# Kernel optimization log

Measured on AMD Instinct MI355X. Metric: run time of the kernel, lower is better.

## Reference

```python
import jax, jax.numpy as jnp
import numpy as np

B, S, E, D, L, H = 8, 1024, 512, 1024, 8, 16
HD = D // H                 # 64
ROT = max(HD // 2, 32)      # 32
FF = 4 * D
FUSED = 3 * D + 2 * FF      # q,k,v,ff,ff_gate
EPS = 1e-5


def layer_norm(x, w, b):
    mu = jnp.mean(x, axis=-1, keepdims=True)
    var = jnp.mean(jnp.square(x - mu), axis=-1, keepdims=True)
    return (x - mu) * jax.lax.rsqrt(var + EPS) * w + b


def gelu(x):  # fused_gelu from source (erf form, constant 1.41421)
    return x * 0.5 * (1.0 + jax.scipy.special.erf(x / 1.41421))


def silu(x):
    return x * jax.nn.sigmoid(x)


def rotate_half(x):
    x1, x2 = jnp.split(x, 2, axis=-1)
    return jnp.concatenate([-x2, x1], axis=-1)


def rope_tables(seq_len):
    inv = 1.0 / (10000.0 ** (jnp.arange(0, ROT, 2, dtype=jnp.float32) / ROT))
    freqs = jnp.arange(seq_len, dtype=jnp.float32)[:, None] * inv[None, :]
    emb = jnp.concatenate([freqs, freqs], axis=-1)  # [S, ROT]
    # source caches sin/cos in bfloat16 (precision=torch.bfloat16)
    sin = jnp.sin(emb).astype(jnp.bfloat16).astype(jnp.float32)[None, None]
    cos = jnp.cos(emb).astype(jnp.bfloat16).astype(jnp.float32)[None, None]
    return sin, cos  # [1,1,S,ROT]


def setup_inputs() -> dict:
    key = jax.random.key(0)
    ks = jax.random.split(key, 24)
    std = 0.02
    inp = {
        "noisy_embeds": jax.random.normal(ks[0], (B, S, E), jnp.float32),
        "cond_embeds": jax.random.normal(ks[1], (B, S, E), jnp.float32),
        "prev_embeds": jax.random.normal(ks[2], (B, S, E), jnp.float32),
        "infill_mask": jax.random.uniform(ks[3], (B, S, 1), jnp.float32),
        "attention_mask": jnp.zeros((B, 1, 1, S), jnp.float32),
        "times": jax.random.uniform(ks[4], (B,), jnp.float32),
        # time embedding params
        "fourier_w": jax.random.normal(ks[5], (D // 2, 1), jnp.float32),
        "t1_w": jax.random.normal(ks[6], (D, D), jnp.float32) * std,
        "t1_b": jnp.zeros((D,), jnp.float32),
        "t2_w": jax.random.normal(ks[7], (D, D), jnp.float32) * std,
        "t2_b": jnp.zeros((D,), jnp.float32),
        # input projection
        "in_w": jax.random.normal(ks[8], (D, 4 * E), jnp.float32) * std,
        "in_b": jnp.zeros((D,), jnp.float32),
        # per-layer (stacked) block params
        "ln_w": jnp.ones((L, D), jnp.float32),
        "ln_b": jnp.zeros((L, D), jnp.float32),
        "cond_w": jax.random.normal(ks[9], (L, 2 * D, D), jnp.float32) * std,
        "cond_b": jnp.zeros((L, 2 * D), jnp.float32),
        "proj_w": jax.random.normal(ks[10], (L, FUSED, D), jnp.float32) * std,
        "attn_w": jax.random.normal(ks[11], (L, D, D), jnp.float32) * std,
        "attn_b": jnp.zeros((L, D), jnp.float32),
        "ff_w": jax.random.normal(ks[12], (L, D, FF), jnp.float32) * std,
        "ff_b": jnp.zeros((L, D), jnp.float32),
        # output head
        "outln_w": jnp.ones((D,), jnp.float32),
        "outln_b": jnp.zeros((D,), jnp.float32),
        "out_w": jax.random.normal(ks[13], (E, D), jnp.float32) * std,
        "out_b": jnp.zeros((E,), jnp.float32),
        "fin_w": jnp.ones((E,), jnp.float32),
        "fin_b": jnp.zeros((E,), jnp.float32),
    }
    return inp


def _split_heads(x):  # [B,S,H*hd] -> [B,H,S,hd]
    return x.reshape(B, S, H, HD).transpose(0, 2, 1, 3)


def _forward(noisy_embeds, cond_embeds, prev_embeds, infill_mask, attention_mask,
             times, fourier_w, t1_w, t1_b, t2_w, t2_b, in_w, in_b,
             ln_w, ln_b, cond_w, cond_b, proj_w, attn_w, attn_b, ff_w, ff_b,
             outln_w, outln_b, out_w, out_b, fin_w, fin_b):
    # -- time embedding (Random Fourier + MLP) --
    f = 2.0 * np.pi * (times[:, None] @ fourier_w.T)          # [B, D/2]
    te = jnp.concatenate([jnp.cos(f), jnp.sin(f)], axis=-1)   # [B, D]
    te = gelu(te @ t1_w.T + t1_b) @ t2_w.T + t2_b             # [B, D]
    time_embeds = te[:, None, :]                              # [B, 1, D]

    # -- input projection: cat(noisy, cond, prev, mask broadcast) --
    mask_feat = infill_mask * jnp.ones_like(noisy_embeds)     # [B,S,E]
    x = jnp.concatenate([noisy_embeds, cond_embeds, prev_embeds, mask_feat], axis=-1)
    h = x @ in_w.T + in_b                                     # [B,S,D]

    sin, cos = rope_tables(S)
    sm_scale = HD ** (-0.5)

    for i in range(L):
        units = layer_norm(h, ln_w[i], ln_b[i])
        # FiLM conditioning
        sb = silu(time_embeds) @ cond_w[i].T + cond_b[i]      # [B,1,2D]
        scale, bias = jnp.split(sb, 2, axis=-1)
        units = (1.0 + scale) * units + bias
        # fused projection and split
        proj = units @ proj_w[i].T                            # [B,S,11D]
        q, k, v, ff, ff_gate = jnp.split(
            proj, np.cumsum([D, D, D, FF])[:4].tolist(), axis=-1)
        q, k, v = _split_heads(q), _split_heads(k), _split_heads(v)  # [B,H,S,hd]
        # rotary on first ROT dims
        q = jnp.concatenate(
            [q[..., :ROT] * cos + rotate_half(q[..., :ROT]) * sin, q[..., ROT:]], axis=-1)
        k = jnp.concatenate(
            [k[..., :ROT] * cos + rotate_half(k[..., :ROT]) * sin, k[..., ROT:]], axis=-1)
        # NOTE: source scales BOTH q and k by hd^-0.5 (effective hd^-1)
        score = jnp.einsum('bhsd,bhSd->bhsS', q * sm_scale, k * sm_scale)
        score = score + attention_mask
        w = jax.nn.softmax(score, axis=-1)
        attn = jnp.einsum('bhsS,bhSd->bhsd', w, v)
        merged = attn.transpose(0, 2, 1, 3).reshape(B, S, D)
        attn_out = merged @ attn_w[i].T + attn_b[i]
        ff_out = (ff * gelu(ff_gate)) @ ff_w[i].T + ff_b[i]
        h = h + attn_out + ff_out

    out = layer_norm(h, outln_w, outln_b) @ out_w.T + out_b   # [B,S,E]
    return layer_norm(out, fin_w, fin_b)


def reference(noisy_embeds, cond_embeds, prev_embeds, infill_mask, attention_mask,
              times, fourier_w, t1_w, t1_b, t2_w, t2_b, in_w, in_b,
              ln_w, ln_b, cond_w, cond_b, proj_w, attn_w, attn_b, ff_w, ff_b,
              outln_w, outln_b, out_w, out_b, fin_w, fin_b):
    return _forward(noisy_embeds, cond_embeds, prev_embeds, infill_mask, attention_mask,
                    times, fourier_w, t1_w, t1_b, t2_w, t2_b, in_w, in_b,
                    ln_w, ln_b, cond_w, cond_b, proj_w, attn_w, attn_b, ff_w, ff_b,
                    outln_w, outln_b, out_w, out_b, fin_w, fin_b)
```

## Files before the change

### kernel.cpp

```cpp
#include <hip/hip_runtime.h>
#include <hip/hip_bf16.h>
#include <cstddef>
#include <cstdint>

#define BB 8
#define SS 1024
#define EE 512
#define DD 1024
#define LL 8
#define HH 16
#define HD 64
#define ROT 32
#define FF 4096
#define FUSED 11264
#define NTOK 8192
#define QKVW 3072

using u16 = unsigned short;
typedef __attribute__((ext_vector_type(8))) __bf16 bf16x8;
typedef __attribute__((ext_vector_type(4))) float f32x4;
typedef __attribute__((ext_vector_type(4))) unsigned short u16x4;
typedef __attribute__((ext_vector_type(8))) unsigned short u16x8;

typedef const __attribute__((address_space(1))) void gas_t;
typedef __attribute__((address_space(3))) void las_t;

__device__ __forceinline__ void gld16(const void* g, void* l) {
  __builtin_amdgcn_global_load_lds((gas_t*)g, (las_t*)l, 16, 0, 0);
}

__device__ __forceinline__ float bf2f(u16 u) {
  union { unsigned int i; float f; } v; v.i = ((unsigned int)u) << 16; return v.f;
}
__device__ __forceinline__ u16 f2bf(float f) {
  union { float f; unsigned int i; } v; v.f = f;
  unsigned int u = v.i;
  unsigned int r = u + 0x7FFFu + ((u >> 16) & 1u);
  return (u16)(r >> 16);
}
__device__ __forceinline__ float gelu_f(float x) {
  return x * 0.5f * (1.0f + erff(x / 1.41421f));
}
__device__ __forceinline__ float silu_f(float x) {
  return x / (1.0f + __expf(-x));
}

template <int ACCUM, int OUTBF16, int GATED>
__global__ __launch_bounds__(256, 2) void gemm_bt(
    const u16* __restrict__ A, const u16* __restrict__ W,
    const float* __restrict__ bias, void* __restrict__ Cp,
    int M, int N, int K) {
  __shared__ __align__(16) u16 As[2][128 * 64];
  __shared__ __align__(16) u16 Bs[2][128 * 64];
  const int tid = threadIdx.x;
  const int w = tid >> 6, lane = tid & 63;
  const int m0 = blockIdx.y * 128, n0 = blockIdx.x * 128;
  const int wm = w >> 1, wn = w & 1;

  f32x4 acc[4][4] = {};

  auto stage = [&](int buf, int k0) {
#pragma unroll
    for (int i = 0; i < 4; i++) {
      const int c = w + i * 4;
      const int r = c * 8 + (lane >> 3);
      const int colb = ((lane & 7) << 4) ^ ((r & 7) << 4);
      gld16(A + (size_t)(m0 + r) * K + k0 + (colb >> 1), &As[buf][c * 512]);
      gld16(W + (size_t)(n0 + r) * K + k0 + (colb >> 1), &Bs[buf][c * 512]);
    }
  };

  stage(0, 0);
  __syncthreads();

  for (int k0 = 0; k0 < K; k0 += 64) {
    const int cur = (k0 >> 6) & 1;
    if (k0 + 64 < K) stage(cur ^ 1, k0 + 64);

    __builtin_amdgcn_s_setprio(1);
#pragma unroll
    for (int ks = 0; ks < 2; ks++) {
      bf16x8 av[4], bv[4];
#pragma unroll
      for (int m = 0; m < 4; m++) {
        const int row = wm * 64 + m * 16 + (lane & 15);
        const int cb = (ks * 64 + ((lane >> 4) << 4)) ^ ((row & 7) << 4);
        av[m] = *(const bf16x8*)((const char*)As[cur] + row * 128 + cb);
      }
#pragma unroll
      for (int n = 0; n < 4; n++) {
        const int row = wn * 64 + n * 16 + (lane & 15);
        const int cb = (ks * 64 + ((lane >> 4) << 4)) ^ ((row & 7) << 4);
        bv[n] = *(const bf16x8*)((const char*)Bs[cur] + row * 128 + cb);
      }
#pragma unroll
      for (int m = 0; m < 4; m++)
#pragma unroll
        for (int n = 0; n < 4; n++)
          acc[m][n] = __builtin_amdgcn_mfma_f32_16x16x32_bf16(av[m], bv[n], acc[m][n], 0, 0, 0);
    }
    __builtin_amdgcn_s_setprio(0);
    __syncthreads();
  }

  const int rowb0 = m0 + wm * 64 + ((lane >> 4) << 2);
  if (GATED) {
    const int No = N >> 1;
#pragma unroll
    for (int n = 0; n < 4; n += 2) {
      const int outcol = (n0 >> 1) + wn * 32 + ((n >> 1) << 4) + (lane & 15);
#pragma unroll
      for (int m = 0; m < 4; m++)
#pragma unroll
        for (int r = 0; r < 4; r++) {
          const float fv = acc[m][n][r];
          const float gv = acc[m][n + 1][r];
          ((u16*)Cp)[(size_t)(rowb0 + m * 16 + r) * No + outcol] = f2bf(fv * gelu_f(gv));
        }
    }
    return;
  }
  const int colb0 = n0 + wn * 64 + (lane & 15);
#pragma unroll
  for (int n = 0; n < 4; n++) {
    const int col = colb0 + n * 16;
    const float bn = bias ? bias[col] : 0.0f;
#pragma unroll
    for (int m = 0; m < 4; m++) {
#pragma unroll
      for (int r = 0; r < 4; r++) {
        const size_t idx = (size_t)(rowb0 + m * 16 + r) * N + col;
        const float v = acc[m][n][r] + bn;
        if (ACCUM) {
          ((float*)Cp)[idx] += v;
        } else if (OUTBF16) {
          ((u16*)Cp)[idx] = f2bf(v);
        } else {
          ((float*)Cp)[idx] = v;
        }
      }
    }
  }
}

__global__ __launch_bounds__(256, 2) void attn_fwd(
    const u16* __restrict__ qr, const u16* __restrict__ kr,
    const u16* __restrict__ vt, const float* __restrict__ mask,
    u16* __restrict__ merged) {
  __shared__ __align__(16) u16 Ks[2][128 * 64];
  __shared__ __align__(16) u16 Vs[2][64 * 128];
  __shared__ __align__(16) u16 Ps[4][16 * 128];
  const int tid = threadIdx.x, w = tid >> 6, lane = tid & 63;
  const int g = blockIdx.x;
  const int j = g >> 3;
  const int bh = (g & 7) + ((j >> 4) << 3);
  const int qx = j & 15;
  const int b = bh >> 4;
  const int q0 = qx * 64 + w * 16;
  const u16* Qb = qr + (size_t)bh * SS * HD;
  const u16* Kb = kr + (size_t)bh * SS * HD;
  const u16* Vb = vt + (size_t)bh * HD * SS;
  const float* mb = mask + (size_t)b * SS;

  bf16x8 qf0, qf1;
  {
    const int qrow = q0 + (lane & 15);
    const u16* qp = Qb + (size_t)qrow * HD + ((lane >> 4) << 3);
    qf0 = *(const bf16x8*)qp;
    qf1 = *(const bf16x8*)(qp + 32);
  }

  float mrun[4], srun[4];
  f32x4 acc[4] = {};
#pragma unroll
  for (int r = 0; r < 4; r++) { mrun[r] = -1e30f; srun[r] = 0.0f; }

  u16* pw = &Ps[w][0];

  auto stage = [&](int buf, int kv0) {
#pragma unroll
    for (int i = 0; i < 4; i++) {
      const int c = w + i * 4;
      {
        const int r = c * 8 + (lane >> 3);
        const int colb = ((lane & 7) << 4) ^ ((r & 7) << 4);
        gld16(Kb + (size_t)(kv0 + r) * HD + (colb >> 1), &Ks[buf][c * 512]);
      }
      {
        const int d = c * 4 + (lane >> 4);
        const int colb = ((lane & 15) << 4) ^ ((d & 7) << 4);
        gld16(Vb + (size_t)d * SS + kv0 + (colb >> 1), &Vs[buf][c * 512]);
      }
    }
  };

  stage(0, 0);
  __syncthreads();

  for (int t = 0; t < 8; t++) {
    const int cur = t & 1;
    const int kv0 = t * 128;
    if (t < 7) stage(cur ^ 1, kv0 + 128);

    f32x4 p[8];
    __builtin_amdgcn_s_setprio(1);
#pragma unroll
    for (int blk = 0; blk < 8; blk++) {
      const int row = blk * 16 + (lane & 15);
      const int swz = (row & 7) << 4;
      const bf16x8 k0v = *(const bf16x8*)((const char*)Ks[cur] + row * 128 + ((((lane >> 4) << 4)) ^ swz));
      const bf16x8 k1v = *(const bf16x8*)((const char*)Ks[cur] + row * 128 + ((64 + ((lane >> 4) << 4)) ^ swz));
      f32x4 z = {};
      p[blk] = __builtin_amdgcn_mfma_f32_16x16x32_bf16(qf0, k0v, z, 0, 0, 0);
      p[blk] = __builtin_amdgcn_mfma_f32_16x16x32_bf16(qf1, k1v, p[blk], 0, 0, 0);
    }
    __builtin_amdgcn_s_setprio(0);

    float mv[8];
#pragma unroll
    for (int blk = 0; blk < 8; blk++) mv[blk] = mb[kv0 + blk * 16 + (lane & 15)];
#pragma unroll
    for (int blk = 0; blk < 8; blk++)
#pragma unroll
      for (int r = 0; r < 4; r++) p[blk][r] = p[blk][r] * (1.0f / 64.0f) + mv[blk];

    float fac[4];
#pragma unroll
    for (int r = 0; r < 4; r++) {
      float tm = p[0][r];
#pragma unroll
      for (int blk = 1; blk < 8; blk++) tm = fmaxf(tm, p[blk][r]);
      tm = fmaxf(tm, __shfl_xor(tm, 1));
      tm = fmaxf(tm, __shfl_xor(tm, 2));
      tm = fmaxf(tm, __shfl_xor(tm, 4));
      tm = fmaxf(tm, __shfl_xor(tm, 8));
      const float mn = fmaxf(mrun[r], tm);
      fac[r] = __expf(mrun[r] - mn);
      mrun[r] = mn;
      float rs = 0.0f;
#pragma unroll
      for (int blk = 0; blk < 8; blk++) {
        const float e = __expf(p[blk][r] - mn);
        p[blk][r] = e;
        rs += e;
      }
      rs += __shfl_xor(rs, 1);
      rs += __shfl_xor(rs, 2);
      rs += __shfl_xor(rs, 4);
      rs += __shfl_xor(rs, 8);
      srun[r] = srun[r] * fac[r] + rs;
    }
#pragma unroll
    for (int dblk = 0; dblk < 4; dblk++)
#pragma unroll
      for (int r = 0; r < 4; r++) acc[dblk][r] *= fac[r];

#pragma unroll
    for (int blk = 0; blk < 8; blk++)
#pragma unroll
      for (int r = 0; r < 4; r++) {
        const int q = ((lane >> 4) << 2) + r;
        pw[(q * 128 + blk * 16 + (lane & 15)) ^ ((q & 7) << 3)] = f2bf(p[blk][r]);
      }

    bf16x8 pa[4];
#pragma unroll
    for (int ks = 0; ks < 4; ks++) {
      const int q = lane & 15;
      pa[ks] = *(const bf16x8*)(pw + ((q * 128 + ks * 32 + ((lane >> 4) << 3)) ^ ((q & 7) << 3)));
    }

    __builtin_amdgcn_s_setprio(1);
#pragma unroll
    for (int dblk = 0; dblk < 4; dblk++) {
      const int drow = dblk * 16 + (lane & 15);
      const int swz = (drow & 7) << 4;
#pragma unroll
      for (int ks = 0; ks < 4; ks++) {
        const bf16x8 vv = *(const bf16x8*)((const char*)Vs[cur] + drow * 256 + ((ks * 64 + ((lane >> 4) << 4)) ^ swz));
        acc[dblk] = __builtin_amdgcn_mfma_f32_16x16x32_bf16(pa[ks], vv, acc[dblk], 0, 0, 0);
      }
    }
    __builtin_amdgcn_s_setprio(0);

    __syncthreads();
  }

#pragma unroll
  for (int dblk = 0; dblk < 4; dblk++)
#pragma unroll
    for (int r = 0; r < 4; r++) {
      const int sq = q0 + ((lane >> 4) << 2) + r;
      const int d = dblk * 16 + (lane & 15);
      merged[((size_t)b * SS + sq) * DD + (bh & 15) * HD + d] = f2bf(acc[dblk][r] / srun[r]);
    }
}

__global__ __launch_bounds__(256) void ln_mod(
    const float* __restrict__ x, const float* __restrict__ lw,
    const float* __restrict__ lb, const float* __restrict__ sb,
    u16* __restrict__ out) {
  const int row = blockIdx.x, tid = threadIdx.x;
  const float4 v = ((const float4*)(x + (size_t)row * DD))[tid];
  float vv[4] = {v.x, v.y, v.z, v.w};
  float s = vv[0] + vv[1] + vv[2] + vv[3];
  float q = vv[0] * vv[0] + vv[1] * vv[1] + vv[2] * vv[2] + vv[3] * vv[3];
  for (int off = 1; off < 64; off <<= 1) {
    s += __shfl_xor(s, off);
    q += __shfl_xor(q, off);
  }
  __shared__ float red[8];
  const int w = tid >> 6, lane = tid & 63;
  if (lane == 0) { red[w] = s; red[4 + w] = q; }
  __syncthreads();
  s = red[0] + red[1] + red[2] + red[3];
  q = red[4] + red[5] + red[6] + red[7];
  const float mu = s * (1.0f / DD);
  const float inv = rsqrtf(q * (1.0f / DD) - mu * mu + 1e-5f);
  const int b = row >> 10;
  u16x4 o;
#pragma unroll
  for (int j = 0; j < 4; j++) {
    const int d = tid * 4 + j;
    float g = (vv[j] - mu) * inv * lw[d] + lb[d];
    if (sb) g = (1.0f + sb[(size_t)b * 2048 + d]) * g + sb[(size_t)b * 2048 + DD + d];
    o[j] = f2bf(g);
  }
  *(u16x4*)(out + (size_t)row * DD + tid * 4) = o;
}

__global__ __launch_bounds__(128) void ln_fin(
    const float* __restrict__ x, const float* __restrict__ w_,
    const float* __restrict__ b_, float* __restrict__ out) {
  const int row = blockIdx.x, tid = threadIdx.x;
  const float4 v = ((const float4*)(x + (size_t)row * EE))[tid];
  float vv[4] = {v.x, v.y, v.z, v.w};
  float s = vv[0] + vv[1] + vv[2] + vv[3];
  float q = vv[0] * vv[0] + vv[1] * vv[1] + vv[2] * vv[2] + vv[3] * vv[3];
  for (int off = 1; off < 64; off <<= 1) {
    s += __shfl_xor(s, off);
    q += __shfl_xor(q, off);
  }
  __shared__ float red[4];
  const int w = tid >> 6, lane = tid & 63;
  if (lane == 0) { red[w] = s; red[2 + w] = q; }
  __syncthreads();
  s = red[0] + red[1];
  q = red[2] + red[3];
  const float mu = s * (1.0f / EE);
  const float inv = rsqrtf(q * (1.0f / EE) - mu * mu + 1e-5f);
  float4 o;
  o.x = (vv[0] - mu) * inv * w_[tid * 4 + 0] + b_[tid * 4 + 0];
  o.y = (vv[1] - mu) * inv * w_[tid * 4 + 1] + b_[tid * 4 + 1];
  o.z = (vv[2] - mu) * inv * w_[tid * 4 + 2] + b_[tid * 4 + 2];
  o.w = (vv[3] - mu) * inv * w_[tid * 4 + 3] + b_[tid * 4 + 3];
  ((float4*)(out + (size_t)row * EE))[tid] = o;
}

template <int IA, int OA>
__global__ __launch_bounds__(256) void vec_gemm(
    const float* __restrict__ in, const float* __restrict__ W,
    const float* __restrict__ bias, float* __restrict__ out, int N, int K) {
  const int n = blockIdx.x * 256 + threadIdx.x;
  const int b = blockIdx.y, l = blockIdx.z;
  const float* ir = in + (size_t)b * K;
  const float* wr = W + ((size_t)l * N + n) * K;
  float s = bias[(size_t)l * N + n];
  for (int k = 0; k < K; k += 4) {
    float4 a = *(const float4*)(ir + k);
    const float4 ww = *(const float4*)(wr + k);
    if (IA) { a.x = silu_f(a.x); a.y = silu_f(a.y); a.z = silu_f(a.z); a.w = silu_f(a.w); }
    s += a.x * ww.x + a.y * ww.y + a.z * ww.z + a.w * ww.w;
  }
  if (OA) s = gelu_f(s);
  out[((size_t)l * gridDim.y + b) * N + n] = s;
}

__global__ void time_fourier(const float* __restrict__ times,
                             const float* __restrict__ fw, float* __restrict__ te0) {
  const int j = blockIdx.x * 256 + threadIdx.x;
  const int b = blockIdx.y;
  const float f = 6.28318530717958647692f * times[b] * fw[j];
  te0[(size_t)b * DD + j] = cosf(f);
  te0[(size_t)b * DD + 512 + j] = sinf(f);
}

__global__ void rope_tab(float* __restrict__ st, float* __restrict__ ct) {
  const int s = blockIdx.x;
  const int j = threadIdx.x;
  const int i = j & 15;
  const float inv = powf(10000.0f, -(float)i * (1.0f / 16.0f));
  const float f = (float)s * inv;
  st[s * 32 + j] = bf2f(f2bf(sinf(f)));
  ct[s * 32 + j] = bf2f(f2bf(cosf(f)));
}

__global__ void build_x(const float* __restrict__ a, const float* __restrict__ b,
                        const float* __restrict__ c, const float* __restrict__ m,
                        u16* __restrict__ x) {
  const size_t i4 = ((size_t)blockIdx.x * 256 + threadIdx.x) * 4;
  if (i4 >= (size_t)NTOK * 2048) return;
  const size_t tok = i4 >> 11;
  const int e = (int)(i4 & 2047);
  float4 v;
  if (e < 512)       v = *(const float4*)(a + tok * 512 + e);
  else if (e < 1024) v = *(const float4*)(b + tok * 512 + (e - 512));
  else if (e < 1536) v = *(const float4*)(c + tok * 512 + (e - 1024));
  else { const float mm = m[tok]; v = make_float4(mm, mm, mm, mm); }
  u16x4 o;
  o[0] = f2bf(v.x); o[1] = f2bf(v.y); o[2] = f2bf(v.z); o[3] = f2bf(v.w);
  *(u16x4*)(x + i4) = o;
}

__global__ void rope_qk(const u16* __restrict__ proj, const float* __restrict__ st,
                        const float* __restrict__ ct, u16* __restrict__ q,
                        u16* __restrict__ k) {
  const size_t idx = (size_t)blockIdx.x * 256 + threadIdx.x;
  const size_t tok = idx >> 10;
  const int hd = (int)(idx & 1023);
  const int hh = hd >> 6, d = hd & 63;
  const int s = (int)(tok & 1023);
  const size_t bb = tok >> 10;
  const u16* pr = proj + tok * QKVW;
  float qv = bf2f(pr[hd]);
  float kv = bf2f(pr[DD + hd]);
  if (d < ROT) {
    const float cs = ct[s * 32 + d], sn = st[s * 32 + d];
    const int pidx = hd - d + ((d < 16) ? d + 16 : d - 16);
    const float qp = bf2f(pr[pidx]);
    const float kp = bf2f(pr[DD + pidx]);
    const float sg = (d < 16) ? -1.0f : 1.0f;
    qv = qv * cs + sg * qp * sn;
    kv = kv * cs + sg * kp * sn;
  }
  const size_t o = ((bb * HH + hh) * SS + s) * HD + d;
  q[o] = f2bf(qv);
  k[o] = f2bf(kv);
}

__global__ __launch_bounds__(256) void transp_v(const u16* __restrict__ proj,
                                                u16* __restrict__ v) {
  __shared__ u16 tile[64 * 72];
  const int tid = threadIdx.x;
  const int s0 = blockIdx.x * 64, h = blockIdx.y, b = blockIdx.z;
  {
    const int sl = tid >> 2, qd = (tid & 3) * 16;
    const u16* src = proj + (size_t)(b * SS + s0 + sl) * QKVW + 2 * DD + h * 64 + qd;
    const u16x8 a0 = *(const u16x8*)src;
    const u16x8 a1 = *(const u16x8*)(src + 8);
    *(u16x8*)&tile[sl * 72 + qd] = a0;
    *(u16x8*)&tile[sl * 72 + qd + 8] = a1;
  }
  __syncthreads();
  {
    const int dl = tid >> 2, qs = (tid & 3) * 16;
    u16x8 o0, o1;
#pragma unroll
    for (int j = 0; j < 8; j++) o0[j] = tile[(qs + j) * 72 + dl];
#pragma unroll
    for (int j = 0; j < 8; j++) o1[j] = tile[(qs + 8 + j) * 72 + dl];
    u16* dst = v + ((size_t)(b * HH + h) * HD + dl) * SS + s0 + qs;
    *(u16x8*)dst = o0;
    *(u16x8*)(dst + 8) = o1;
  }
}

__global__ void cast_bf16(const float* __restrict__ in, u16* __restrict__ out, size_t n4) {
  const size_t i = (size_t)blockIdx.x * 256 + threadIdx.x;
  if (i >= n4) return;
  const float4 v = ((const float4*)in)[i];
  u16x4 o;
  o[0] = f2bf(v.x); o[1] = f2bf(v.y); o[2] = f2bf(v.z); o[3] = f2bf(v.w);
  ((u16x4*)out)[i] = o;
}

__global__ void cast_q(const float* __restrict__ src, u16* __restrict__ dst) {
  const int i = blockIdx.x * 256 + threadIdx.x;
  const int l = blockIdx.y;
  const int r = i >> 7, cb = (i & 127) * 8;
  const float* s = src + ((size_t)l * FUSED + r) * DD + cb;
  const float4 a = *(const float4*)s;
  const float4 b = *(const float4*)(s + 4);
  u16x8 o;
  o[0] = f2bf(a.x); o[1] = f2bf(a.y); o[2] = f2bf(a.z); o[3] = f2bf(a.w);
  o[4] = f2bf(b.x); o[5] = f2bf(b.y); o[6] = f2bf(b.z); o[7] = f2bf(b.w);
  *(u16x8*)(dst + ((size_t)l * QKVW + r) * DD + cb) = o;
}

__global__ void cast_ffg(const float* __restrict__ src, u16* __restrict__ dst) {
  const int i = blockIdx.x * 256 + threadIdx.x;
  const int l = blockIdx.y;
  const int r = i >> 7, cb = (i & 127) * 8;
  const int t16 = r >> 4, pos = r & 15;
  const int j = (t16 >> 1) * 16 + pos;
  const int srow = (t16 & 1) ? (3 * DD + FF + j) : (3 * DD + j);
  const float* s = src + ((size_t)l * FUSED + srow) * DD + cb;
  const float4 a = *(const float4*)s;
  const float4 b = *(const float4*)(s + 4);
  u16x8 o;
  o[0] = f2bf(a.x); o[1] = f2bf(a.y); o[2] = f2bf(a.z); o[3] = f2bf(a.w);
  o[4] = f2bf(b.x); o[5] = f2bf(b.y); o[6] = f2bf(b.z); o[7] = f2bf(b.w);
  *(u16x8*)(dst + ((size_t)l * 8192 + r) * DD + cb) = o;
}

extern "C" void kernel_launch(void* const* d_in, const int* in_sizes, int n_in,
                              void* d_out, int out_size, void* d_ws, size_t ws_size,
                              hipStream_t stream) {
  const float* noisy   = (const float*)d_in[0];
  const float* condi   = (const float*)d_in[1];
  const float* prev    = (const float*)d_in[2];
  const float* infill  = (const float*)d_in[3];
  const float* amask   = (const float*)d_in[4];
  const float* times   = (const float*)d_in[5];
  const float* fourier = (const float*)d_in[6];
  const float* t1_w    = (const float*)d_in[7];
  const float* t1_b    = (const float*)d_in[8];
  const float* t2_w    = (const float*)d_in[9];
  const float* t2_b    = (const float*)d_in[10];
  const float* in_w    = (const float*)d_in[11];
  const float* in_b    = (const float*)d_in[12];
  const float* ln_w    = (const float*)d_in[13];
  const float* ln_b    = (const float*)d_in[14];
  const float* cond_w  = (const float*)d_in[15];
  const float* cond_b  = (const float*)d_in[16];
  const float* proj_w  = (const float*)d_in[17];
  const float* attn_w  = (const float*)d_in[18];
  const float* attn_b  = (const float*)d_in[19];
  const float* ff_w    = (const float*)d_in[20];
  const float* ff_b    = (const float*)d_in[21];
  const float* outln_w = (const float*)d_in[22];
  const float* outln_b = (const float*)d_in[23];
  const float* out_w   = (const float*)d_in[24];
  const float* out_b   = (const float*)d_in[25];
  const float* fin_w   = (const float*)d_in[26];
  const float* fin_b   = (const float*)d_in[27];
  float* outp = (float*)d_out;

  char* p = (char*)d_ws;
  auto alloc = [&](size_t bytes) -> char* {
    char* r = p;
    p += (bytes + 255) & ~(size_t)255;
    return r;
  };
  u16* in_w_h   = (u16*)alloc((size_t)DD * 2048 * 2);
  u16* projq_w_h = (u16*)alloc((size_t)LL * QKVW * DD * 2);
  u16* ffg_w_h  = (u16*)alloc((size_t)LL * 8192 * DD * 2);
  u16* attn_w_h = (u16*)alloc((size_t)LL * DD * DD * 2);
  u16* ff_w_h   = (u16*)alloc((size_t)LL * DD * FF * 2);
  u16* out_w_h  = (u16*)alloc((size_t)EE * DD * 2);
  float* te0 = (float*)alloc((size_t)BB * DD * 4);
  float* te1 = (float*)alloc((size_t)BB * DD * 4);
  float* te2 = (float*)alloc((size_t)BB * DD * 4);
  float* sb  = (float*)alloc((size_t)LL * BB * 2048 * 4);
  float* stab = (float*)alloc((size_t)SS * 32 * 4);
  float* ctab = (float*)alloc((size_t)SS * 32 * 4);
  u16* xb    = (u16*)alloc((size_t)NTOK * 2048 * 2);
  float* h   = (float*)alloc((size_t)NTOK * DD * 4);
  u16* units = (u16*)alloc((size_t)NTOK * DD * 2);
  u16* projq = (u16*)alloc((size_t)NTOK * QKVW * 2);
  u16* qrb   = (u16*)alloc((size_t)NTOK * DD * 2);
  u16* krb   = (u16*)alloc((size_t)NTOK * DD * 2);
  u16* vtb   = (u16*)alloc((size_t)NTOK * DD * 2);
  u16* mg    = (u16*)alloc((size_t)NTOK * DD * 2);
  u16* ffa   = (u16*)alloc((size_t)NTOK * FF * 2);
  u16* hn    = (u16*)alloc((size_t)NTOK * DD * 2);
  float* ob  = (float*)alloc((size_t)NTOK * EE * 4);

  auto castN = [&](const float* src, u16* dst, size_t n) {
    const size_t n4 = n / 4;
    cast_bf16<<<dim3((unsigned)((n4 + 255) / 256)), dim3(256), 0, stream>>>(src, dst, n4);
  };
  castN(in_w, in_w_h, (size_t)DD * 2048);
  cast_q<<<dim3(QKVW * 128 / 256, LL), 256, 0, stream>>>(proj_w, projq_w_h);
  cast_ffg<<<dim3(8192 * 128 / 256, LL), 256, 0, stream>>>(proj_w, ffg_w_h);
  castN(attn_w, attn_w_h, (size_t)LL * DD * DD);
  castN(ff_w, ff_w_h, (size_t)LL * DD * FF);
  castN(out_w, out_w_h, (size_t)EE * DD);

  time_fourier<<<dim3(2, BB), 256, 0, stream>>>(times, fourier, te0);
  vec_gemm<0, 1><<<dim3(4, BB, 1), 256, 0, stream>>>(te0, t1_w, t1_b, te1, 1024, 1024);
  vec_gemm<0, 0><<<dim3(4, BB, 1), 256, 0, stream>>>(te1, t2_w, t2_b, te2, 1024, 1024);
  vec_gemm<1, 0><<<dim3(8, BB, LL), 256, 0, stream>>>(te2, cond_w, cond_b, sb, 2048, 1024);
  rope_tab<<<SS, 32, 0, stream>>>(stab, ctab);
  build_x<<<16384, 256, 0, stream>>>(noisy, condi, prev, infill, xb);
  gemm_bt<0, 0, 0><<<dim3(DD / 128, NTOK / 128), 256, 0, stream>>>(xb, in_w_h, in_b, h, NTOK, DD, 2048);

  for (int l = 0; l < LL; l++) {
    ln_mod<<<NTOK, 256, 0, stream>>>(h, ln_w + (size_t)l * DD, ln_b + (size_t)l * DD,
                                     sb + (size_t)l * BB * 2048, units);
    gemm_bt<0, 1, 0><<<dim3(QKVW / 128, NTOK / 128), 256, 0, stream>>>(
        units, projq_w_h + (size_t)l * QKVW * DD, nullptr, projq, NTOK, QKVW, DD);
    gemm_bt<0, 0, 1><<<dim3(8192 / 128, NTOK / 128), 256, 0, stream>>>(
        units, ffg_w_h + (size_t)l * 8192 * DD, nullptr, ffa, NTOK, 8192, DD);
    rope_qk<<<32768, 256, 0, stream>>>(projq, stab, ctab, qrb, krb);
    transp_v<<<dim3(SS / 64, HH, BB), 256, 0, stream>>>(projq, vtb);
    attn_fwd<<<dim3(2048), 256, 0, stream>>>(qrb, krb, vtb, amask, mg);
    gemm_bt<1, 0, 0><<<dim3(DD / 128, NTOK / 128), 256, 0, stream>>>(
        mg, attn_w_h + (size_t)l * DD * DD, attn_b + (size_t)l * DD, h, NTOK, DD, DD);
    gemm_bt<1, 0, 0><<<dim3(DD / 128, NTOK / 128), 256, 0, stream>>>(
        ffa, ff_w_h + (size_t)l * DD * FF, ff_b + (size_t)l * DD, h, NTOK, DD, FF);
  }

  ln_mod<<<NTOK, 256, 0, stream>>>(h, outln_w, outln_b, nullptr, hn);
  gemm_bt<0, 0, 0><<<dim3(EE / 128, NTOK / 128), 256, 0, stream>>>(hn, out_w_h, out_b, ob, NTOK, EE, DD);
  ln_fin<<<NTOK, 128, 0, stream>>>(ob, fin_w, fin_b, outp);
}
```

Before: 5.125 ms.

## Deepen GEMM prefetch pipeline and add 256x256 tile kernel for gated FF

The main bf16 GEMM now preloads two K-tiles, reads both halves of the LDS tile into registers up front, and issues the next global-to-LDS stage in the middle of the MFMA work, so loads overlap compute better. A new 512-thread 256x256-tile GEMM variant replaces the gated FF/gate projection, the largest GEMM, to raise arithmetic intensity per byte loaded. The larger kernel uses 128 KB of LDS per block and many more accumulator registers, which may limit occupancy, and the shared buffer is overwritten while the second half is still being computed from registers.

```diff
diff --git a/kernel.cpp b/kernel.cpp
--- a/kernel.cpp
+++ b/kernel.cpp
@@ -45,7 +45,7 @@
   return x / (1.0f + __expf(-x));
 }
 
-template <int ACCUM, int OUTBF16, int GATED>
+template <int ACCUM, int OUTBF16>
 __global__ __launch_bounds__(256, 2) void gemm_bt(
     const u16* __restrict__ A, const u16* __restrict__ W,
     const float* __restrict__ bias, void* __restrict__ Cp,
@@ -70,56 +70,48 @@
     }
   };
 
+  const int nt = K >> 6;
   stage(0, 0);
+  stage(1, 64);
   __syncthreads();
 
-  for (int k0 = 0; k0 < K; k0 += 64) {
-    const int cur = (k0 >> 6) & 1;
-    if (k0 + 64 < K) stage(cur ^ 1, k0 + 64);
-
+  for (int t = 0; t < nt; t++) {
+    const int cur = t & 1;
+    bf16x8 av0[4], bv0[4], av1[4], bv1[4];
+#pragma unroll
+    for (int m = 0; m < 4; m++) {
+      const int row = wm * 64 + m * 16 + (lane & 15);
+      const int sw = (row & 7) << 4;
+      av0[m] = *(const bf16x8*)((const char*)As[cur] + row * 128 + ((((lane >> 4) << 4)) ^ sw));
+      av1[m] = *(const bf16x8*)((const char*)As[cur] + row * 128 + ((64 + ((lane >> 4) << 4)) ^ sw));
+    }
+#pragma unroll
+    for (int n = 0; n < 4; n++) {
+      const int row = wn * 64 + n * 16 + (lane & 15);
+      const int sw = (row & 7) << 4;
+      bv0[n] = *(const bf16x8*)((const char*)Bs[cur] + row * 128 + ((((lane >> 4) << 4)) ^ sw));
+      bv1[n] = *(const bf16x8*)((const char*)Bs[cur] + row * 128 + ((64 + ((lane >> 4) << 4)) ^ sw));
+    }
     __builtin_amdgcn_s_setprio(1);
 #pragma unroll
-    for (int ks = 0; ks < 2; ks++) {
-      bf16x8 av[4], bv[4];
-#pragma unroll
-      for (int m = 0; m < 4; m++) {
-        const int row = wm * 64 + m * 16 + (lane & 15);
-        const int cb = (ks * 64 + ((lane >> 4) << 4)) ^ ((row & 7) << 4);
-        av[m] = *(const bf16x8*)((const char*)As[cur] + row * 128 + cb);
-      }
-#pragma unroll
-      for (int n = 0; n < 4; n++) {
-        const int row = wn * 64 + n * 16 + (lane & 15);
-        const int cb = (ks * 64 + ((lane >> 4) << 4)) ^ ((row & 7) << 4);
-        bv[n] = *(const bf16x8*)((const char*)Bs[cur] + row * 128 + cb);
-      }
-#pragma unroll
-      for (int m = 0; m < 4; m++)
-#pragma unroll
-        for (int n = 0; n < 4; n++)
-          acc[m][n] = __builtin_amdgcn_mfma_f32_16x16x32_bf16(av[m], bv[n], acc[m][n], 0, 0, 0);
-    }
+    for (int m = 0; m < 4; m++)
+#pragma unroll
+      for (int n = 0; n < 4; n++)
+        acc[m][n] = __builtin_amdgcn_mfma_f32_16x16x32_bf16(av0[m], bv0[n], acc[m][n], 0, 0, 0);
     __builtin_amdgcn_s_setprio(0);
+    __builtin_amdgcn_sched_barrier(0);
     __syncthreads();
+    if (t + 2 < nt) stage(cur, (t + 2) << 6);
+    __builtin_amdgcn_s_setprio(1);
+#pragma unroll
+    for (int m = 0; m < 4; m++)
+#pragma unroll
+      for (int n = 0; n < 4; n++)
+        acc[m][n] = __builtin_amdgcn_mfma_f32_16x16x32_bf16(av1[m], bv1[n], acc[m][n], 0, 0, 0);
+    __builtin_amdgcn_s_setprio(0);
   }
 
   const int rowb0 = m0 + wm * 64 + ((lane >> 4) << 2);
-  if (GATED) {
-    const int No = N >> 1;
-#pragma unroll
-    for (int n = 0; n < 4; n += 2) {
-      const int outcol = (n0 >> 1) + wn * 32 + ((n >> 1) << 4) + (lane & 15);
-#pragma unroll
-      for (int m = 0; m < 4; m++)
-#pragma unroll
-        for (int r = 0; r < 4; r++) {
-          const float fv = acc[m][n][r];
-          const float gv = acc[m][n + 1][r];
-          ((u16*)Cp)[(size_t)(rowb0 + m * 16 + r) * No + outcol] = f2bf(fv * gelu_f(gv));
-        }
-    }
-    return;
-  }
   const int colb0 = n0 + wn * 64 + (lane & 15);
 #pragma unroll
   for (int n = 0; n < 4; n++) {
@@ -139,6 +131,113 @@
           ((float*)Cp)[idx] = v;
         }
       }
+    }
+  }
+}
+
+template <int GATED>
+__global__ __launch_bounds__(512, 2) void gemm_bt256(
+    const u16* __restrict__ A, const u16* __restrict__ W,
+    void* __restrict__ Cp, int M, int N, int K) {
+  __shared__ __align__(16) u16 As[2][256 * 64];
+  __shared__ __align__(16) u16 Bs[2][256 * 64];
+  const int tid = threadIdx.x;
+  const int w = tid >> 6, lane = tid & 63;
+  const int m0 = blockIdx.y * 256, n0 = blockIdx.x * 256;
+  const int wm = w >> 2, wn = w & 3;
+
+  f32x4 acc[8][4] = {};
+
+  auto stage = [&](int buf, int k0) {
+#pragma unroll
+    for (int i = 0; i < 4; i++) {
+      const int c = w + i * 8;
+      const int r = c * 8 + (lane >> 3);
+      const int colb = ((lane & 7) << 4) ^ ((r & 7) << 4);
+      gld16(A + (size_t)(m0 + r) * K + k0 + (colb >> 1), &As[buf][c * 512]);
+      gld16(W + (size_t)(n0 + r) * K + k0 + (colb >> 1), &Bs[buf][c * 512]);
+    }
+  };
+
+  const int nt = K >> 6;
+  stage(0, 0);
+  stage(1, 64);
+  __syncthreads();
+
+  for (int t = 0; t < nt; t++) {
+    const int cur = t & 1;
+    {
+      bf16x8 av0[8], bv0[4];
+#pragma unroll
+      for (int m = 0; m < 8; m++) {
+        const int row = wm * 128 + m * 16 + (lane & 15);
+        const int cb = (((lane >> 4) << 4)) ^ ((row & 7) << 4);
+        av0[m] = *(const bf16x8*)((const char*)As[cur] + row * 128 + cb);
+      }
+#pragma unroll
+      for (int n = 0; n < 4; n++) {
+        const int row = wn * 64 + n * 16 + (lane & 15);
+        const int cb = (((lane >> 4) << 4)) ^ ((row & 7) << 4);
+        bv0[n] = *(const bf16x8*)((const char*)Bs[cur] + row * 128 + cb);
+      }
+      __builtin_amdgcn_s_setprio(1);
+#pragma unroll
+      for (int m = 0; m < 8; m++)
+#pragma unroll
+        for (int n = 0; n < 4; n++)
+          acc[m][n] = __builtin_amdgcn_mfma_f32_16x16x32_bf16(av0[m], bv0[n], acc[m][n], 0, 0, 0);
+      __builtin_amdgcn_s_setprio(0);
+    }
+    bf16x8 av1[8], bv1[4];
+#pragma unroll
+    for (int m = 0; m < 8; m++) {
+      const int row = wm * 128 + m * 16 + (lane & 15);
+      const int cb = (64 + ((lane >> 4) << 4)) ^ ((row & 7) << 4);
+      av1[m] = *(const bf16x8*)((const char*)As[cur] + row * 128 + cb);
+    }
+#pragma unroll
+    for (int n = 0; n < 4; n++) {
+      const int row = wn * 64 + n * 16 + (lane & 15);
+      const int cb = (64 + ((lane >> 4) << 4)) ^ ((row & 7) << 4);
+      bv1[n] = *(const bf16x8*)((const char*)Bs[cur] + row * 128 + cb);
+    }
+    __builtin_amdgcn_sched_barrier(0);
+    __syncthreads();
+    if (t + 2 < nt) stage(cur, (t + 2) << 6);
+    __builtin_amdgcn_s_setprio(1);
+#pragma unroll
+    for (int m = 0; m < 8; m++)
+#pragma unroll
+      for (int n = 0; n < 4; n++)
+        acc[m][n] = __builtin_amdgcn_mfma_f32_16x16x32_bf16(av1[m], bv1[n], acc[m][n], 0, 0, 0);
+    __builtin_amdgcn_s_setprio(0);
+  }
+
+  const int rowb0 = m0 + wm * 128 + ((lane >> 4) << 2);
+  if (GATED) {
+    const int No = N >> 1;
+#pragma unroll
+    for (int n = 0; n < 4; n += 2) {
+      const int outcol = (n0 >> 1) + wn * 32 + ((n >> 1) << 4) + (lane & 15);
+#pragma unroll
+      for (int m = 0; m < 8; m++)
+#pragma unroll
+        for (int r = 0; r < 4; r++) {
+          const float fv = acc[m][n][r];
+          const float gv = acc[m][n + 1][r];
+          ((u16*)Cp)[(size_t)(rowb0 + m * 16 + r) * No + outcol] = f2bf(fv * gelu_f(gv));
+        }
+    }
+  } else {
+    const int colb0 = n0 + wn * 64 + (lane & 15);
+#pragma unroll
+    for (int n = 0; n < 4; n++) {
+      const int col = colb0 + n * 16;
+#pragma unroll
+      for (int m = 0; m < 8; m++)
+#pragma unroll
+        for (int r = 0; r < 4; r++)
+          ((u16*)Cp)[(size_t)(rowb0 + m * 16 + r) * N + col] = f2bf(acc[m][n][r]);
     }
   }
 }
@@ -583,25 +682,25 @@
   vec_gemm<1, 0><<<dim3(8, BB, LL), 256, 0, stream>>>(te2, cond_w, cond_b, sb, 2048, 1024);
   rope_tab<<<SS, 32, 0, stream>>>(stab, ctab);
   build_x<<<16384, 256, 0, stream>>>(noisy, condi, prev, infill, xb);
-  gemm_bt<0, 0, 0><<<dim3(DD / 128, NTOK / 128), 256, 0, stream>>>(xb, in_w_h, in_b, h, NTOK, DD, 2048);
+  gemm_bt<0, 0><<<dim3(DD / 128, NTOK / 128), 256, 0, stream>>>(xb, in_w_h, in_b, h, NTOK, DD, 2048);
 
   for (int l = 0; l < LL; l++) {
     ln_mod<<<NTOK, 256, 0, stream>>>(h, ln_w + (size_t)l * DD, ln_b + (size_t)l * DD,
                                      sb + (size_t)l * BB * 2048, units);
-    gemm_bt<0, 1, 0><<<dim3(QKVW / 128, NTOK / 128), 256, 0, stream>>>(
+    gemm_bt<0, 1><<<dim3(QKVW / 128, NTOK / 128), 256, 0, stream>>>(
         units, projq_w_h + (size_t)l * QKVW * DD, nullptr, projq, NTOK, QKVW, DD);
-    gemm_bt<0, 0, 1><<<dim3(8192 / 128, NTOK / 128), 256, 0, stream>>>(
-        units, ffg_w_h + (size_t)l * 8192 * DD, nullptr, ffa, NTOK, 8192, DD);
+    gemm_bt256<1><<<dim3(8192 / 256, NTOK / 256), 512, 0, stream>>>(
+        units, ffg_w_h + (size_t)l * 8192 * DD, ffa, NTOK, 8192, DD);
     rope_qk<<<32768, 256, 0, stream>>>(projq, stab, ctab, qrb, krb);
     transp_v<<<dim3(SS / 64, HH, BB), 256, 0, stream>>>(projq, vtb);
     attn_fwd<<<dim3(2048), 256, 0, stream>>>(qrb, krb, vtb, amask, mg);
-    gemm_bt<1, 0, 0><<<dim3(DD / 128, NTOK / 128), 256, 0, stream>>>(
+    gemm_bt<1, 0><<<dim3(DD / 128, NTOK / 128), 256, 0, stream>>>(
         mg, attn_w_h + (size_t)l * DD * DD, attn_b + (size_t)l * DD, h, NTOK, DD, DD);
-    gemm_bt<1, 0, 0><<<dim3(DD / 128, NTOK / 128), 256, 0, stream>>>(
+    gemm_bt<1, 0><<<dim3(DD / 128, NTOK / 128), 256, 0, stream>>>(
         ffa, ff_w_h + (size_t)l * DD * FF, ff_b + (size_t)l * DD, h, NTOK, DD, FF);
   }
 
   ln_mod<<<NTOK, 256, 0, stream>>>(h, outln_w, outln_b, nullptr, hn);
-  gemm_bt<0, 0, 0><<<dim3(EE / 128, NTOK / 128), 256, 0, stream>>>(hn, out_w_h, out_b, ob, NTOK, EE, DD);
+  gemm_bt<0, 0><<<dim3(EE / 128, NTOK / 128), 256, 0, stream>>>(hn, out_w_h, out_b, ob, NTOK, EE, DD);
   ln_fin<<<NTOK, 128, 0, stream>>>(ob, fin_w, fin_b, outp);
 }
```

New measurement: 4.882 ms. 4.7% less time.
